# Kernel optimization log

Measured on AMD Instinct MI355X. Metric: run time of the kernel, lower is better.

Reference implementation:

```python
import jax, jax.numpy as jnp
import numpy as np

N = 50000      # nodes
E = 800000     # edges (avg degree 16)
F_IN = 512     # num_feature
H = 256        # nhid


def setup_inputs() -> dict:
    key = jax.random.key(0)
    ks = jax.random.split(key, 40)
    def p(k, shape):
        return jax.random.normal(k, shape, jnp.float32) * 0.05
    inp = {}
    inp["x"] = jax.random.normal(ks[0], (N, F_IN), jnp.float32)
    src = jax.random.randint(ks[1], (E,), 0, N, jnp.int32)
    dst = jax.random.randint(ks[2], (E,), 0, N, jnp.int32)
    inp["edge_index"] = jnp.stack([src, dst])  # [2, E]
    # GIN conv MLPs: Lin(din,H), ReLU, Lin(H,H). Weights stored [in, out].
    dims = [F_IN, H, H, H]
    i = 3
    for li, din in enumerate(dims, 1):
        inp[f"c{li}w1"] = p(ks[i], (din, H)); i += 1
        inp[f"c{li}b1"] = p(ks[i], (H,)); i += 1
        inp[f"c{li}w2"] = p(ks[i], (H, H)); i += 1
        inp[f"c{li}b2"] = p(ks[i], (H,)); i += 1
    # 2-layer LSTM, gate order i,f,g,o; single fused bias (b_ih + b_hh).
    for l in range(2):
        inp[f"lstm{l}_wih"] = p(ks[i], (H, 4 * H)); i += 1
        inp[f"lstm{l}_whh"] = p(ks[i], (H, 4 * H)); i += 1
        inp[f"lstm{l}_b"] = p(ks[i], (4 * H,)); i += 1
    inp["mlp_w"] = p(ks[i], (H, H)); i += 1
    inp["mlp_b"] = p(ks[i], (H,))
    return inp


def _gin(h, src, dst, w1, b1, w2, b2):
    # GINConv with eps=0: nn(x + sum_{j->i} x_j)
    agg = jax.ops.segment_sum(h[src], dst, num_segments=N)
    z = jax.nn.relu((h + agg) @ w1 + b1)
    return z @ w2 + b2


def _lstm_layer(seq, wih, whh, b):
    # seq: [T, N, H] -> hidden states [T, N, H]
    def step(carry, xt):
        h, c = carry
        g = xt @ wih + h @ whh + b
        i, f, gg, o = jnp.split(g, 4, axis=-1)
        c = jax.nn.sigmoid(f) * c + jax.nn.sigmoid(i) * jnp.tanh(gg)
        h = jax.nn.sigmoid(o) * jnp.tanh(c)
        return (h, c), h
    h0 = jnp.zeros((seq.shape[1], whh.shape[0]), seq.dtype)
    _, hs = jax.lax.scan(step, (h0, h0), seq)
    return hs


def reference(x, edge_index, c1w1, c1b1, c1w2, c1b2, c2w1, c2b1, c2w2, c2b2,
              c3w1, c3b1, c3w2, c3b2, c4w1, c4b1, c4w2, c4b2,
              lstm0_wih, lstm0_whh, lstm0_b, lstm1_wih, lstm1_whh, lstm1_b,
              mlp_w, mlp_b):
    src, dst = edge_index[0], edge_index[1]
    x1 = jax.nn.relu(_gin(x, src, dst, c1w1, c1b1, c1w2, c1b2))
    x2 = jax.nn.relu(_gin(x1, src, dst, c2w1, c2b1, c2w2, c2b2))
    x3 = jax.nn.relu(_gin(x2, src, dst, c3w1, c3b1, c3w2, c3b2))
    x4 = jax.nn.relu(_gin(x3, src, dst, c4w1, c4b1, c4w2, c4b2))
    # residual sums (in-place cascade as in the original)
    x2 = x2 + x1
    x3 = x3 + x2
    x4 = x4 + x3
    x_sum = x1 + x2 + x3 + x4
    stack = jnp.stack([x_sum, x1, x2, x3, x4])  # [5, N, H]
    x_avg = stack.mean(axis=0)
    x_max = stack.max(axis=0)
    seq = jnp.stack([x1, x2, x3, x4])  # [4, N, H]
    h = _lstm_layer(seq, lstm0_wih, lstm0_whh, lstm0_b)
    h = _lstm_layer(h, lstm1_wih, lstm1_whh, lstm1_b)
    x_lstm = h.mean(axis=0)
    # channel attention: relu(mlp(x_avg) + mlp(x_max) + mlp(x_lstm))
    return jax.nn.relu((x_avg + x_max + x_lstm) @ mlp_w + 3.0 * mlp_b)
```

## Files before the change

kernel.cpp:

```cpp
#include <hip/hip_runtime.h>

typedef unsigned int u32;
typedef unsigned short u16;

typedef __attribute__((ext_vector_type(8))) __bf16 bf16x8;
typedef __attribute__((ext_vector_type(4))) float f32x4;

__device__ __forceinline__ u16 f2bf(float f) {
  u32 u = __float_as_uint(f);
  u += 0x7fffu + ((u >> 16) & 1u);
  return (u16)(u >> 16);
}
__device__ __forceinline__ float bl(u32 u) { return __uint_as_float(u << 16); }
__device__ __forceinline__ float bh(u32 u) { return __uint_as_float(u & 0xffff0000u); }
__device__ __forceinline__ u32 pk2(float a, float b) { return (u32)f2bf(a) | ((u32)f2bf(b) << 16); }
__device__ __forceinline__ float fsig(float x) { return 1.f / (1.f + __expf(-x)); }
__device__ __forceinline__ float ftanh(float x) { return 1.f - 2.f / (__expf(2.f * x) + 1.f); }

#define GLDS16(gp, lp)                                                                  \
  __builtin_amdgcn_global_load_lds((const __attribute__((address_space(1))) u32*)(gp),  \
                                   (__attribute__((address_space(3))) u32*)(lp), 16, 0, 0)

struct WTargs {
  const float* src[13];
  u16* dst[13];
  int K[13];
  int Nc[13];
  int bstart[14];
};
__global__ __launch_bounds__(256) void k_wtall(WTargs wa) {
  int b = blockIdx.x;
  int w = 0;
  while (b >= wa.bstart[w + 1]) ++w;
  int i = (b - wa.bstart[w]) * 256 + threadIdx.x;
  int K = wa.K[w], Nc = wa.Nc[w];
  if (i >= K * Nc) return;
  int k = i / Nc, c = i - k * Nc;
  wa.dst[w][(size_t)c * K + k] = f2bf(wa.src[w][i]);
}

__global__ __launch_bounds__(256) void k_x2bf(const float* __restrict__ x, u16* __restrict__ xb, int total8) {
  int i = blockIdx.x * 256 + threadIdx.x;
  if (i >= total8) return;
  size_t o = (size_t)i * 8;
  float4 a = *(const float4*)(x + o), b = *(const float4*)(x + o + 4);
  uint4 v;
  v.x = pk2(a.x, a.y); v.y = pk2(a.z, a.w); v.z = pk2(b.x, b.y); v.w = pk2(b.z, b.w);
  *(uint4*)(xb + o) = v;
}

__global__ void k_hist(const int* __restrict__ dst, int* __restrict__ deg, int E) {
  int e = blockIdx.x * 256 + threadIdx.x;
  if (e < E) atomicAdd(&deg[dst[e]], 1);
}
__global__ __launch_bounds__(1024) void k_scan1(const int* __restrict__ deg, int* __restrict__ rs,
                                                int* __restrict__ bsum, int n) {
  __shared__ int buf[1024];
  int t = threadIdx.x, idx = blockIdx.x * 1024 + t;
  int v = idx < n ? deg[idx] : 0;
  buf[t] = v;
  __syncthreads();
  for (int off = 1; off < 1024; off <<= 1) {
    int u = t >= off ? buf[t - off] : 0;
    __syncthreads();
    buf[t] += u;
    __syncthreads();
  }
  if (idx < n) rs[idx + 1] = buf[t];
  if (t == 1023) bsum[blockIdx.x] = buf[1023];
}
__global__ void k_scan2(int* bsum, int nb) {
  if (threadIdx.x == 0) {
    int s = 0;
    for (int b = 0; b < nb; ++b) { s += bsum[b]; bsum[b] = s; }
  }
}
__global__ void k_scan3(const int* __restrict__ bsum, int* __restrict__ rs,
                        int* __restrict__ cursor, int n) {
  int i = blockIdx.x * 256 + threadIdx.x;
  if (i >= n) return;
  int b = i >> 10;
  int add = b ? bsum[b - 1] : 0;
  int v = rs[i + 1] + add;
  int d = cursor[i];
  rs[i + 1] = v;
  cursor[i] = v - d;
  if (i == 0) rs[0] = 0;
}
__global__ void k_scatter(const int* __restrict__ src, const int* __restrict__ dst,
                          int* __restrict__ cursor, int* __restrict__ esrc, int E) {
  int e = blockIdx.x * 256 + threadIdx.x;
  if (e < E) {
    int p = atomicAdd(&cursor[dst[e]], 1);
    esrc[p] = src[e];
  }
}

__global__ __launch_bounds__(256) void k_agg512_bf(const u16* __restrict__ xb,
                                                   const int* __restrict__ rowstart,
                                                   const int* __restrict__ esrc,
                                                   u16* __restrict__ out, int Nn, int base, int rows) {
  int lane = threadIdx.x & 63, wid = threadIdx.x >> 6;
  int r = blockIdx.x * 4 + wid;
  if (r >= rows) return;
  int node = base + r;
  const int cb = lane * 8;
  u16* orow = out + (size_t)r * 512 + cb;
  if (node >= Nn) { *(uint4*)orow = uint4{0, 0, 0, 0}; return; }
  float acc[8];
  {
    uint4 v = *(const uint4*)(xb + (size_t)node * 512 + cb);
    acc[0] = bl(v.x); acc[1] = bh(v.x); acc[2] = bl(v.y); acc[3] = bh(v.y);
    acc[4] = bl(v.z); acc[5] = bh(v.z); acc[6] = bl(v.w); acc[7] = bh(v.w);
  }
  int s = rowstart[node], e = rowstart[node + 1];
  int j = s;
  for (; j + 3 < e; j += 4) {
    uint4 v0 = *(const uint4*)(xb + (size_t)esrc[j] * 512 + cb);
    uint4 v1 = *(const uint4*)(xb + (size_t)esrc[j + 1] * 512 + cb);
    uint4 v2 = *(const uint4*)(xb + (size_t)esrc[j + 2] * 512 + cb);
    uint4 v3 = *(const uint4*)(xb + (size_t)esrc[j + 3] * 512 + cb);
    acc[0] += (bl(v0.x) + bl(v1.x)) + (bl(v2.x) + bl(v3.x));
    acc[1] += (bh(v0.x) + bh(v1.x)) + (bh(v2.x) + bh(v3.x));
    acc[2] += (bl(v0.y) + bl(v1.y)) + (bl(v2.y) + bl(v3.y));
    acc[3] += (bh(v0.y) + bh(v1.y)) + (bh(v2.y) + bh(v3.y));
    acc[4] += (bl(v0.z) + bl(v1.z)) + (bl(v2.z) + bl(v3.z));
    acc[5] += (bh(v0.z) + bh(v1.z)) + (bh(v2.z) + bh(v3.z));
    acc[6] += (bl(v0.w) + bl(v1.w)) + (bl(v2.w) + bl(v3.w));
    acc[7] += (bh(v0.w) + bh(v1.w)) + (bh(v2.w) + bh(v3.w));
  }
  for (; j < e; ++j) {
    uint4 v = *(const uint4*)(xb + (size_t)esrc[j] * 512 + cb);
    acc[0] += bl(v.x); acc[1] += bh(v.x); acc[2] += bl(v.y); acc[3] += bh(v.y);
    acc[4] += bl(v.z); acc[5] += bh(v.z); acc[6] += bl(v.w); acc[7] += bh(v.w);
  }
  uint4 o;
  o.x = pk2(acc[0], acc[1]); o.y = pk2(acc[2], acc[3]);
  o.z = pk2(acc[4], acc[5]); o.w = pk2(acc[6], acc[7]);
  *(uint4*)orow = o;
}

__global__ __launch_bounds__(256) void k_agg256(const u16* __restrict__ h,
                                                const int* __restrict__ rowstart,
                                                const int* __restrict__ esrc,
                                                u16* __restrict__ out, int Nn, int base, int rows) {
  int lane = threadIdx.x & 63, wid = threadIdx.x >> 6;
  int r = blockIdx.x * 4 + wid;
  if (r >= rows) return;
  int node = base + r;
  const int cb = lane * 4;
  u16* orow = out + (size_t)r * 256 + cb;
  if (node >= Nn) { *(uint2*)orow = uint2{0, 0}; return; }
  float acc[4];
  {
    uint2 v = *(const uint2*)(h + (size_t)node * 256 + cb);
    acc[0] = bl(v.x); acc[1] = bh(v.x); acc[2] = bl(v.y); acc[3] = bh(v.y);
  }
  int s = rowstart[node], e = rowstart[node + 1];
  int j = s;
  for (; j + 3 < e; j += 4) {
    uint2 v0 = *(const uint2*)(h + (size_t)esrc[j] * 256 + cb);
    uint2 v1 = *(const uint2*)(h + (size_t)esrc[j + 1] * 256 + cb);
    uint2 v2 = *(const uint2*)(h + (size_t)esrc[j + 2] * 256 + cb);
    uint2 v3 = *(const uint2*)(h + (size_t)esrc[j + 3] * 256 + cb);
    acc[0] += (bl(v0.x) + bl(v1.x)) + (bl(v2.x) + bl(v3.x));
    acc[1] += (bh(v0.x) + bh(v1.x)) + (bh(v2.x) + bh(v3.x));
    acc[2] += (bl(v0.y) + bl(v1.y)) + (bl(v2.y) + bl(v3.y));
    acc[3] += (bh(v0.y) + bh(v1.y)) + (bh(v2.y) + bh(v3.y));
  }
  for (; j < e; ++j) {
    uint2 v = *(const uint2*)(h + (size_t)esrc[j] * 256 + cb);
    acc[0] += bl(v.x); acc[1] += bh(v.x); acc[2] += bl(v.y); acc[3] += bh(v.y);
  }
  uint2 o;
  o.x = pk2(acc[0], acc[1]); o.y = pk2(acc[2], acc[3]);
  *(uint2*)orow = o;
}

template <int BN, int MODE>
__global__ __launch_bounds__(256) void k_gemm(const u16* __restrict__ A1, const u16* __restrict__ B1, int K1,
                                              const u16* __restrict__ A2, const u16* __restrict__ B2, int K2,
                                              const float* __restrict__ bias, float bscale,
                                              void* __restrict__ outp, int Nout, int Mstore,
                                              float* __restrict__ cstp, float* __restrict__ hsump,
                                              int first, int dosum) {
  constexpr int NF = BN / 32;
  __shared__ u16 Al[128 * 64];
  __shared__ u16 Bl[BN * 64];
  const int tid = threadIdx.x;
  const int lane = tid & 63, wid = tid >> 6;
  const int wr = wid >> 1, wc = wid & 1;
  const int m0 = blockIdx.x * 128;
  const int n0 = blockIdx.y * BN;
  const int h0 = blockIdx.y * 32;
  const int l15 = lane & 15, l4 = lane >> 4;
  const int srow = lane >> 3, scol = (lane & 7) * 8;
  f32x4 acc[4][NF] = {};

  for (int s = 0; s < 2; ++s) {
    const u16* A = s ? A2 : A1;
    const u16* B = s ? B2 : B1;
    const int K = s ? K2 : K1;
    if (A == nullptr) continue;
    for (int k0 = 0; k0 < K; k0 += 64) {
      __syncthreads();
#pragma unroll
      for (int p = 0; p < 4; ++p) {
        int r = m0 + p * 32 + wid * 8 + srow;
        GLDS16(A + (size_t)r * K + k0 + scol, &Al[(p * 32 + wid * 8) * 64]);
      }
#pragma unroll
      for (int p = 0; p < NF; ++p) {
        int r;
        if constexpr (MODE == 3) r = p * 256 + h0 + wid * 8 + srow;
        else r = n0 + p * 32 + wid * 8 + srow;
        GLDS16(B + (size_t)r * K + k0 + scol, &Bl[(p * 32 + wid * 8) * 64]);
      }
      __syncthreads();
#pragma unroll
      for (int ks = 0; ks < 2; ++ks) {
        const int kk = ks * 32 + l4 * 8;
        bf16x8 af[4], bfr[NF];
#pragma unroll
        for (int m = 0; m < 4; ++m)
          af[m] = *(const bf16x8*)&Al[(wr * 64 + m * 16 + l15) * 64 + kk];
#pragma unroll
        for (int n = 0; n < NF; ++n) {
          int trow;
          if constexpr (MODE == 3) trow = n * 32 + wc * 16 + l15;
          else trow = wc * (BN / 2) + n * 16 + l15;
          bfr[n] = *(const bf16x8*)&Bl[trow * 64 + kk];
        }
#pragma unroll
        for (int m = 0; m < 4; ++m)
#pragma unroll
          for (int n = 0; n < NF; ++n)
            acc[m][n] = __builtin_amdgcn_mfma_f32_16x16x32_bf16(af[m], bfr[n], acc[m][n], 0, 0, 0);
      }
    }
  }

  if constexpr (MODE == 3) {
    const int hcol = h0 + wc * 16 + l15;
    const float bi = bias[hcol], bf2 = bias[256 + hcol];
    const float bg = bias[512 + hcol], bo = bias[768 + hcol];
    u16* hout = (u16*)outp;
#pragma unroll
    for (int m = 0; m < 4; ++m) {
      int gr0 = m0 + wr * 64 + m * 16 + l4 * 4;
#pragma unroll
      for (int r = 0; r < 4; ++r) {
        int gr = gr0 + r;
        if (gr >= Mstore) continue;
        float gi = acc[m][0][r] + bi;
        float gf = acc[m][1][r] + bf2;
        float gg = acc[m][2][r] + bg;
        float go = acc[m][3][r] + bo;
        size_t o = (size_t)gr * 256 + hcol;
        float nc = fsig(gi) * ftanh(gg);
        if (!first) nc += fsig(gf) * cstp[o];
        cstp[o] = nc;
        float h = fsig(go) * ftanh(nc);
        hout[o] = f2bf(h);
        if (dosum) {
          if (first) hsump[o] = h;
          else hsump[o] += h;
        }
      }
    }
    return;
  }

#pragma unroll
  for (int m = 0; m < 4; ++m) {
    int gr0 = m0 + wr * 64 + m * 16 + l4 * 4;
#pragma unroll
    for (int n = 0; n < NF; ++n) {
      int gc = n0 + wc * (BN / 2) + n * 16 + l15;
      float bb = bias ? bias[gc] * bscale : 0.f;
#pragma unroll
      for (int r = 0; r < 4; ++r) {
        int gr = gr0 + r;
        if (gr >= Mstore) continue;
        float v = acc[m][n][r] + bb;
        if (MODE >= 1) v = fmaxf(v, 0.f);
        if (MODE == 2) ((float*)outp)[(size_t)gr * Nout + gc] = v;
        else ((u16*)outp)[(size_t)gr * Nout + gc] = f2bf(v);
      }
    }
  }
}

__global__ __launch_bounds__(256) void k_cascade(const u16* __restrict__ x1, u16* __restrict__ x2,
                                                 u16* __restrict__ x3, u16* __restrict__ x4, int total4) {
  int i = blockIdx.x * 256 + threadIdx.x;
  if (i >= total4) return;
  size_t o = (size_t)i * 4;
  uint2 v1 = *(const uint2*)(x1 + o), v2 = *(const uint2*)(x2 + o);
  uint2 v3 = *(const uint2*)(x3 + o), v4 = *(const uint2*)(x4 + o);
  float a1[4] = {bl(v1.x), bh(v1.x), bl(v1.y), bh(v1.y)};
  float a2[4] = {bl(v2.x), bh(v2.x), bl(v2.y), bh(v2.y)};
  float a3[4] = {bl(v3.x), bh(v3.x), bl(v3.y), bh(v3.y)};
  float a4[4] = {bl(v4.x), bh(v4.x), bl(v4.y), bh(v4.y)};
  float y2[4], y3[4], y4[4];
#pragma unroll
  for (int j = 0; j < 4; ++j) {
    y2[j] = a2[j] + a1[j];
    y3[j] = a3[j] + y2[j];
    y4[j] = a4[j] + y3[j];
  }
  *(uint2*)(x2 + o) = uint2{pk2(y2[0], y2[1]), pk2(y2[2], y2[3])};
  *(uint2*)(x3 + o) = uint2{pk2(y3[0], y3[1]), pk2(y3[2], y3[3])};
  *(uint2*)(x4 + o) = uint2{pk2(y4[0], y4[1]), pk2(y4[2], y4[3])};
}

__global__ __launch_bounds__(256) void k_sfin(const u16* __restrict__ x1, const u16* __restrict__ x2,
                                              const u16* __restrict__ x3, const u16* __restrict__ x4,
                                              const float* __restrict__ hsum, u16* __restrict__ sb,
                                              int total4) {
  int i = blockIdx.x * 256 + threadIdx.x;
  if (i >= total4) return;
  size_t o = (size_t)i * 4;
  uint2 v1 = *(const uint2*)(x1 + o), v2 = *(const uint2*)(x2 + o);
  uint2 v3 = *(const uint2*)(x3 + o), v4 = *(const uint2*)(x4 + o);
  float4 hh = *(const float4*)(hsum + o);
  float r0 = 1.4f * (bl(v1.x) + bl(v2.x) + bl(v3.x) + bl(v4.x)) + 0.25f * hh.x;
  float r1 = 1.4f * (bh(v1.x) + bh(v2.x) + bh(v3.x) + bh(v4.x)) + 0.25f * hh.y;
  float r2 = 1.4f * (bl(v1.y) + bl(v2.y) + bl(v3.y) + bl(v4.y)) + 0.25f * hh.z;
  float r3 = 1.4f * (bh(v1.y) + bh(v2.y) + bh(v3.y) + bh(v4.y)) + 0.25f * hh.w;
  *(uint2*)(sb + o) = uint2{pk2(r0, r1), pk2(r2, r3)};
}

extern "C" void kernel_launch(void* const* d_in, const int* in_sizes, int n_in,
                              void* d_out, int out_size, void* d_ws, size_t ws_size,
                              hipStream_t stream) {
  (void)n_in; (void)out_size;
  const int N = in_sizes[0] / 512;
  const int E = in_sizes[1] / 2;
  const int Mpad = ((N + 127) / 128) * 128;
  auto al128 = [](int v) { return ((v + 127) / 128) * 128; };

  const float* x = (const float*)d_in[0];
  const int* ei = (const int*)d_in[1];
  const int* esrc_in = ei;
  const int* edst_in = ei + E;

  size_t off = 0;
  auto alloc = [&](size_t bytes) { size_t o = off; off += (bytes + 255) & ~(size_t)255; return o; };
  char* ws = (char*)d_ws;
  const size_t szH = (size_t)Mpad * 256 * 2;
  const int widx[13] = {2, 4, 6, 8, 10, 12, 14, 16, 18, 19, 21, 22, 24};
  const int wK[13] = {512, 256, 256, 256, 256, 256, 256, 256, 256, 256, 256, 256, 256};
  const int wN[13] = {256, 256, 256, 256, 256, 256, 256, 256, 1024, 1024, 1024, 1024, 256};
  size_t wt_o[13];
  for (int i = 0; i < 13; ++i) wt_o[i] = alloc((size_t)wK[i] * wN[i] * 2);
  size_t rowstart_o = alloc((size_t)(N + 1) * 4);
  size_t cursor_o = alloc((size_t)N * 4);
  size_t bsum_o = alloc(256 * 4);
  size_t esrc_o = alloc((size_t)E * 4);
  size_t xb_o = alloc((size_t)Mpad * 512 * 2);
  size_t x_o[4];
  for (int t = 0; t < 4; ++t) x_o[t] = alloc(szH);
  int McC = al128((Mpad + 3) / 4);
  int McL = al128((Mpad + 7) / 8);
  {
    const int ccand[3] = {Mpad, al128((Mpad + 1) / 2), al128((Mpad + 3) / 4)};
    const int lcand[4] = {al128((Mpad + 1) / 2), 16384, 8192, al128((Mpad + 7) / 8)};
    bool done = false;
    for (int ci = 0; ci < 3 && !done; ++ci) {
      for (int li = 0; li < 4 && !done; ++li) {
        size_t cneed = (size_t)ccand[ci] * 1536;
        size_t lneed = (size_t)lcand[li] * 5632;
        size_t tmp = cneed > lneed ? cneed : lneed;
        if (off + tmp + (1u << 20) <= ws_size) { McC = ccand[ci]; McL = lcand[li]; done = true; }
      }
    }
  }
  const size_t hb = (size_t)McL * 256 * 2;
  const size_t fb = (size_t)McL * 256 * 4;
  size_t lstm_sz = 7 * hb + 2 * fb;
  size_t conv_sz = (size_t)McC * 1536;
  size_t tmp_o = alloc(lstm_sz > conv_sz ? lstm_sz : conv_sz);
  if (off > ws_size) return;

  u16* wt[13];
  for (int i = 0; i < 13; ++i) wt[i] = (u16*)(ws + wt_o[i]);
  int* rowstart = (int*)(ws + rowstart_o);
  int* cursor = (int*)(ws + cursor_o);
  int* bsum = (int*)(ws + bsum_o);
  int* esrc = (int*)(ws + esrc_o);
  u16* xb = (u16*)(ws + xb_o);
  u16* xl[4];
  for (int t = 0; t < 4; ++t) xl[t] = (u16*)(ws + x_o[t]);
  u16* h0s[4];
  for (int t = 0; t < 4; ++t) h0s[t] = (u16*)(ws + tmp_o + t * hb);
  u16* h1p[2] = {(u16*)(ws + tmp_o + 4 * hb), (u16*)(ws + tmp_o + 5 * hb)};
  float* cst = (float*)(ws + tmp_o + 6 * hb);
  float* hsum = (float*)(ws + tmp_o + 6 * hb + fb);
  u16* sbc = (u16*)(ws + tmp_o + 6 * hb + 2 * fb);
  u16* aggC = (u16*)(ws + tmp_o);
  u16* zC = (u16*)(ws + tmp_o + (size_t)McC * 512 * 2);

  WTargs wa;
  int bacc = 0;
  for (int i = 0; i < 13; ++i) {
    wa.src[i] = (const float*)d_in[widx[i]];
    wa.dst[i] = wt[i];
    wa.K[i] = wK[i];
    wa.Nc[i] = wN[i];
    wa.bstart[i] = bacc;
    bacc += (wK[i] * wN[i] + 255) / 256;
  }
  wa.bstart[13] = bacc;
  k_wtall<<<bacc, 256, 0, stream>>>(wa);
  k_x2bf<<<(N * 64 + 255) / 256, 256, 0, stream>>>(x, xb, N * 64);
  hipMemsetAsync(cursor, 0, (size_t)N * 4, stream);
  k_hist<<<(E + 255) / 256, 256, 0, stream>>>(edst_in, cursor, E);
  const int nb = (N + 1023) / 1024;
  k_scan1<<<nb, 1024, 0, stream>>>(cursor, rowstart, bsum, N);
  k_scan2<<<1, 64, 0, stream>>>(bsum, nb);
  k_scan3<<<(N + 255) / 256, 256, 0, stream>>>(bsum, rowstart, cursor, N);
  k_scatter<<<(E + 255) / 256, 256, 0, stream>>>(esrc_in, edst_in, cursor, esrc, E);

  auto gemm = [&](const u16* A1, const u16* B1, int K1, const u16* A2, const u16* B2, int K2,
                  const float* bias, float bscale, void* out, int Nout, int rows, int Mstore,
                  int mode) {
    dim3 b(256);
    if (mode == 0) {
      dim3 g(rows / 128, Nout / 128);
      k_gemm<128, 0><<<g, b, 0, stream>>>(A1, B1, K1, A2, B2, K2, bias, bscale, out, Nout, Mstore,
                                          nullptr, nullptr, 0, 0);
    } else if (mode == 1) {
      dim3 g(rows / 128, Nout / 128);
      k_gemm<128, 1><<<g, b, 0, stream>>>(A1, B1, K1, A2, B2, K2, bias, bscale, out, Nout, Mstore,
                                          nullptr, nullptr, 0, 0);
    } else {
      dim3 g(rows / 128, Nout / 64);
      k_gemm<64, 2><<<g, b, 0, stream>>>(A1, B1, K1, A2, B2, K2, bias, bscale, out, Nout, Mstore,
                                         nullptr, nullptr, 0, 0);
    }
  };
  auto lstm_step = [&](const u16* xt, const u16* wih, const u16* hprev, const u16* whh,
                       const float* bias, u16* hout, float* hsumP, int rows, int first, int dosum) {
    dim3 g(rows / 128, 8), b(256);
    k_gemm<128, 3><<<g, b, 0, stream>>>(xt, wih, 256, hprev, whh, 256, bias, 1.f,
                                        hout, 256, rows, cst, hsumP, first, dosum);
  };

  const u16* cin[4] = {nullptr, xl[0], xl[1], xl[2]};
  u16* cout[4] = {xl[0], xl[1], xl[2], xl[3]};
  const int cb1[4] = {3, 7, 11, 15}, cb2[4] = {5, 9, 13, 17};
  for (int l = 0; l < 4; ++l) {
    const int Kin = l == 0 ? 512 : 256;
    for (int base = 0; base < Mpad; base += McC) {
      int rows = Mpad - base < McC ? Mpad - base : McC;
      int ab = (rows + 3) / 4;
      if (l == 0)
        k_agg512_bf<<<ab, 256, 0, stream>>>(xb, rowstart, esrc, aggC, N, base, rows);
      else
        k_agg256<<<ab, 256, 0, stream>>>(cin[l], rowstart, esrc, aggC, N, base, rows);
      gemm(aggC, wt[2 * l], Kin, nullptr, nullptr, 0, (const float*)d_in[cb1[l]], 1.f,
           zC, 256, rows, rows, 1);
      gemm(zC, wt[2 * l + 1], 256, nullptr, nullptr, 0, (const float*)d_in[cb2[l]], 1.f,
           cout[l] + (size_t)base * 256, 256, rows, rows, 1);
    }
  }
  k_cascade<<<(Mpad * 64 + 255) / 256, 256, 0, stream>>>(xl[0], xl[1], xl[2], xl[3], Mpad * 64);

  const float* b_l0 = (const float*)d_in[20];
  const float* b_l1 = (const float*)d_in[23];
  const float* b_mlp = (const float*)d_in[25];
  for (int base = 0; base < Mpad; base += McL) {
    int rows = Mpad - base < McL ? Mpad - base : McL;
    const size_t boff = (size_t)base * 256;
    for (int t = 0; t < 4; ++t)
      lstm_step(xl[t] + boff, wt[8], t ? h0s[t - 1] : nullptr, wt[9], b_l0,
                h0s[t], nullptr, rows, t == 0, 0);
    for (int t = 0; t < 4; ++t)
      lstm_step(h0s[t], wt[10], t ? h1p[(t + 1) & 1] : nullptr, wt[11], b_l1,
                h1p[t & 1], hsum, rows, t == 0, 1);
    k_sfin<<<(rows * 64 + 255) / 256, 256, 0, stream>>>(xl[0] + boff, xl[1] + boff, xl[2] + boff,
                                                        xl[3] + boff, hsum, sbc, rows * 64);
    int st = N - base;
    if (st > rows) st = rows;
    if (st > 0)
      gemm(sbc, wt[12], 256, nullptr, nullptr, 0, b_mlp, 3.f,
           (float*)d_out + boff, 256, rows, st, 2);
  }
}
```

Measured before the change: 1.755 ms.

## Apply first GIN linear before aggregation and store LSTM cell state in bf16

Layer 1 now multiplies x by W1 first (512->256) and then aggregates the 256-wide projected features, fusing bias and ReLU into the aggregation kernel. This uses linearity of the sum to halve the gather bandwidth of the widest aggregation. Separately, the LSTM cell state is kept in bf16 instead of fp32, which halves its traffic but adds rounding error. Workspace layout is reshuffled so the bf16 copy of x lives in the temporary region, with zero padding via memset.

```diff
diff --git a/kernel.cpp b/kernel.cpp
--- a/kernel.cpp
+++ b/kernel.cpp
@@ -96,48 +96,45 @@
   }
 }
 
-__global__ __launch_bounds__(256) void k_agg512_bf(const u16* __restrict__ xb,
-                                                   const int* __restrict__ rowstart,
-                                                   const int* __restrict__ esrc,
-                                                   u16* __restrict__ out, int Nn, int base, int rows) {
+__global__ __launch_bounds__(256) void k_aggbr(const u16* __restrict__ y, const int* __restrict__ rowstart,
+                                               const int* __restrict__ esrc, const float* __restrict__ b1,
+                                               u16* __restrict__ z, int Nn, int base, int rows) {
   int lane = threadIdx.x & 63, wid = threadIdx.x >> 6;
   int r = blockIdx.x * 4 + wid;
   if (r >= rows) return;
   int node = base + r;
-  const int cb = lane * 8;
-  u16* orow = out + (size_t)r * 512 + cb;
-  if (node >= Nn) { *(uint4*)orow = uint4{0, 0, 0, 0}; return; }
-  float acc[8];
+  const int cb = lane * 4;
+  u16* orow = z + (size_t)r * 256 + cb;
+  if (node >= Nn) { *(uint2*)orow = uint2{0, 0}; return; }
+  float acc[4];
   {
-    uint4 v = *(const uint4*)(xb + (size_t)node * 512 + cb);
+    uint2 v = *(const uint2*)(y + (size_t)node * 256 + cb);
     acc[0] = bl(v.x); acc[1] = bh(v.x); acc[2] = bl(v.y); acc[3] = bh(v.y);
-    acc[4] = bl(v.z); acc[5] = bh(v.z); acc[6] = bl(v.w); acc[7] = bh(v.w);
   }
   int s = rowstart[node], e = rowstart[node + 1];
   int j = s;
   for (; j + 3 < e; j += 4) {
-    uint4 v0 = *(const uint4*)(xb + (size_t)esrc[j] * 512 + cb);
-    uint4 v1 = *(const uint4*)(xb + (size_t)esrc[j + 1] * 512 + cb);
-    uint4 v2 = *(const uint4*)(xb + (size_t)esrc[j + 2] * 512 + cb);
-    uint4 v3 = *(const uint4*)(xb + (size_t)esrc[j + 3] * 512 + cb);
+    uint2 v0 = *(const uint2*)(y + (size_t)esrc[j] * 256 + cb);
+    uint2 v1 = *(const uint2*)(y + (size_t)esrc[j + 1] * 256 + cb);
+    uint2 v2 = *(const uint2*)(y + (size_t)esrc[j + 2] * 256 + cb);
+    uint2 v3 = *(const uint2*)(y + (size_t)esrc[j + 3] * 256 + cb);
     acc[0] += (bl(v0.x) + bl(v1.x)) + (bl(v2.x) + bl(v3.x));
     acc[1] += (bh(v0.x) + bh(v1.x)) + (bh(v2.x) + bh(v3.x));
     acc[2] += (bl(v0.y) + bl(v1.y)) + (bl(v2.y) + bl(v3.y));
     acc[3] += (bh(v0.y) + bh(v1.y)) + (bh(v2.y) + bh(v3.y));
-    acc[4] += (bl(v0.z) + bl(v1.z)) + (bl(v2.z) + bl(v3.z));
-    acc[5] += (bh(v0.z) + bh(v1.z)) + (bh(v2.z) + bh(v3.z));
-    acc[6] += (bl(v0.w) + bl(v1.w)) + (bl(v2.w) + bl(v3.w));
-    acc[7] += (bh(v0.w) + bh(v1.w)) + (bh(v2.w) + bh(v3.w));
   }
   for (; j < e; ++j) {
-    uint4 v = *(const uint4*)(xb + (size_t)esrc[j] * 512 + cb);
+    uint2 v = *(const uint2*)(y + (size_t)esrc[j] * 256 + cb);
     acc[0] += bl(v.x); acc[1] += bh(v.x); acc[2] += bl(v.y); acc[3] += bh(v.y);
-    acc[4] += bl(v.z); acc[5] += bh(v.z); acc[6] += bl(v.w); acc[7] += bh(v.w);
-  }
-  uint4 o;
+  }
+  float4 bb = *(const float4*)(b1 + cb);
+  acc[0] = fmaxf(acc[0] + bb.x, 0.f);
+  acc[1] = fmaxf(acc[1] + bb.y, 0.f);
+  acc[2] = fmaxf(acc[2] + bb.z, 0.f);
+  acc[3] = fmaxf(acc[3] + bb.w, 0.f);
+  uint2 o;
   o.x = pk2(acc[0], acc[1]); o.y = pk2(acc[2], acc[3]);
-  o.z = pk2(acc[4], acc[5]); o.w = pk2(acc[6], acc[7]);
-  *(uint4*)orow = o;
+  *(uint2*)orow = o;
 }
 
 __global__ __launch_bounds__(256) void k_agg256(const u16* __restrict__ h,
@@ -182,7 +179,7 @@
                                               const u16* __restrict__ A2, const u16* __restrict__ B2, int K2,
                                               const float* __restrict__ bias, float bscale,
                                               void* __restrict__ outp, int Nout, int Mstore,
-                                              float* __restrict__ cstp, float* __restrict__ hsump,
+                                              u16* __restrict__ cstp, float* __restrict__ hsump,
                                               int first, int dosum) {
   constexpr int NF = BN / 32;
   __shared__ u16 Al[128 * 64];
@@ -258,8 +255,9 @@
         float go = acc[m][3][r] + bo;
         size_t o = (size_t)gr * 256 + hcol;
         float nc = fsig(gi) * ftanh(gg);
-        if (!first) nc += fsig(gf) * cstp[o];
-        cstp[o] = nc;
+        if (!first) nc += fsig(gf) * bl((u32)cstp[o]);
+        cstp[o] = f2bf(nc);
+        nc = bl((u32)f2bf(nc));
         float h = fsig(go) * ftanh(nc);
         hout[o] = f2bf(h);
         if (dosum) {
@@ -349,6 +347,7 @@
   auto alloc = [&](size_t bytes) { size_t o = off; off += (bytes + 255) & ~(size_t)255; return o; };
   char* ws = (char*)d_ws;
   const size_t szH = (size_t)Mpad * 256 * 2;
+  const size_t szXB = (size_t)Mpad * 512 * 2;
   const int widx[13] = {2, 4, 6, 8, 10, 12, 14, 16, 18, 19, 21, 22, 24};
   const int wK[13] = {512, 256, 256, 256, 256, 256, 256, 256, 256, 256, 256, 256, 256};
   const int wN[13] = {256, 256, 256, 256, 256, 256, 256, 256, 1024, 1024, 1024, 1024, 256};
@@ -358,7 +357,6 @@
   size_t cursor_o = alloc((size_t)N * 4);
   size_t bsum_o = alloc(256 * 4);
   size_t esrc_o = alloc((size_t)E * 4);
-  size_t xb_o = alloc((size_t)Mpad * 512 * 2);
   size_t x_o[4];
   for (int t = 0; t < 4; ++t) x_o[t] = alloc(szH);
   int McC = al128((Mpad + 3) / 4);
@@ -369,8 +367,8 @@
     bool done = false;
     for (int ci = 0; ci < 3 && !done; ++ci) {
       for (int li = 0; li < 4 && !done; ++li) {
-        size_t cneed = (size_t)ccand[ci] * 1536;
-        size_t lneed = (size_t)lcand[li] * 5632;
+        size_t cneed = szXB + szH + (size_t)ccand[ci] * 512;
+        size_t lneed = (size_t)lcand[li] * 5120;
         size_t tmp = cneed > lneed ? cneed : lneed;
         if (off + tmp + (1u << 20) <= ws_size) { McC = ccand[ci]; McL = lcand[li]; done = true; }
       }
@@ -378,8 +376,8 @@
   }
   const size_t hb = (size_t)McL * 256 * 2;
   const size_t fb = (size_t)McL * 256 * 4;
-  size_t lstm_sz = 7 * hb + 2 * fb;
-  size_t conv_sz = (size_t)McC * 1536;
+  size_t lstm_sz = 8 * hb + fb;
+  size_t conv_sz = szXB + szH + (size_t)McC * 512;
   size_t tmp_o = alloc(lstm_sz > conv_sz ? lstm_sz : conv_sz);
   if (off > ws_size) return;
 
@@ -389,17 +387,17 @@
   int* cursor = (int*)(ws + cursor_o);
   int* bsum = (int*)(ws + bsum_o);
   int* esrc = (int*)(ws + esrc_o);
-  u16* xb = (u16*)(ws + xb_o);
   u16* xl[4];
   for (int t = 0; t < 4; ++t) xl[t] = (u16*)(ws + x_o[t]);
+  u16* xb = (u16*)(ws + tmp_o);
+  u16* y1 = (u16*)(ws + tmp_o + szXB);
+  u16* zC = (u16*)(ws + tmp_o + szXB + szH);
   u16* h0s[4];
   for (int t = 0; t < 4; ++t) h0s[t] = (u16*)(ws + tmp_o + t * hb);
   u16* h1p[2] = {(u16*)(ws + tmp_o + 4 * hb), (u16*)(ws + tmp_o + 5 * hb)};
-  float* cst = (float*)(ws + tmp_o + 6 * hb);
-  float* hsum = (float*)(ws + tmp_o + 6 * hb + fb);
-  u16* sbc = (u16*)(ws + tmp_o + 6 * hb + 2 * fb);
-  u16* aggC = (u16*)(ws + tmp_o);
-  u16* zC = (u16*)(ws + tmp_o + (size_t)McC * 512 * 2);
+  u16* cst = (u16*)(ws + tmp_o + 6 * hb);
+  u16* sbc = (u16*)(ws + tmp_o + 7 * hb);
+  float* hsum = (float*)(ws + tmp_o + 8 * hb);
 
   WTargs wa;
   int bacc = 0;
@@ -414,6 +412,7 @@
   wa.bstart[13] = bacc;
   k_wtall<<<bacc, 256, 0, stream>>>(wa);
   k_x2bf<<<(N * 64 + 255) / 256, 256, 0, stream>>>(x, xb, N * 64);
+  if (Mpad > N) hipMemsetAsync(xb + (size_t)N * 512, 0, (size_t)(Mpad - N) * 512 * 2, stream);
   hipMemsetAsync(cursor, 0, (size_t)N * 4, stream);
   k_hist<<<(E + 255) / 256, 256, 0, stream>>>(edst_in, cursor, E);
   const int nb = (N + 1023) / 1024;
@@ -447,22 +446,26 @@
                                         hout, 256, rows, cst, hsumP, first, dosum);
   };
 
-  const u16* cin[4] = {nullptr, xl[0], xl[1], xl[2]};
-  u16* cout[4] = {xl[0], xl[1], xl[2], xl[3]};
-  const int cb1[4] = {3, 7, 11, 15}, cb2[4] = {5, 9, 13, 17};
-  for (int l = 0; l < 4; ++l) {
-    const int Kin = l == 0 ? 512 : 256;
+  gemm(xb, wt[0], 512, nullptr, nullptr, 0, nullptr, 0.f, y1, 256, Mpad, Mpad, 0);
+  for (int base = 0; base < Mpad; base += McC) {
+    int rows = Mpad - base < McC ? Mpad - base : McC;
+    int ab = (rows + 3) / 4;
+    k_aggbr<<<ab, 256, 0, stream>>>(y1, rowstart, esrc, (const float*)d_in[3], zC, N, base, rows);
+    gemm(zC, wt[1], 256, nullptr, nullptr, 0, (const float*)d_in[5], 1.f,
+         xl[0] + (size_t)base * 256, 256, rows, rows, 1);
+  }
+  for (int l = 1; l < 4; ++l) {
+    const int cb1[4] = {3, 7, 11, 15}, cb2[4] = {5, 9, 13, 17};
     for (int base = 0; base < Mpad; base += McC) {
       int rows = Mpad - base < McC ? Mpad - base : McC;
       int ab = (rows + 3) / 4;
-      if (l == 0)
-        k_agg512_bf<<<ab, 256, 0, stream>>>(xb, rowstart, esrc, aggC, N, base, rows);
-      else
-        k_agg256<<<ab, 256, 0, stream>>>(cin[l], rowstart, esrc, aggC, N, base, rows);
-      gemm(aggC, wt[2 * l], Kin, nullptr, nullptr, 0, (const float*)d_in[cb1[l]], 1.f,
-           zC, 256, rows, rows, 1);
-      gemm(zC, wt[2 * l + 1], 256, nullptr, nullptr, 0, (const float*)d_in[cb2[l]], 1.f,
-           cout[l] + (size_t)base * 256, 256, rows, rows, 1);
+      k_agg256<<<ab, 256, 0, stream>>>(xl[l - 1], rowstart, esrc, zC, N, base, rows);
+      (void)ab;
+      k_aggbr;
+      gemm((u16*)zC, wt[2 * l], 256, nullptr, nullptr, 0, (const float*)d_in[cb1[l]], 1.f,
+           y1, 256, rows, rows, 1);
+      gemm(y1, wt[2 * l + 1], 256, nullptr, nullptr, 0, (const float*)d_in[cb2[l]], 1.f,
+           xl[l] + (size_t)base * 256, 256, rows, rows, 1);
     }
   }
   k_cascade<<<(Mpad * 64 + 255) / 256, 256, 0, stream>>>(xl[0], xl[1], xl[2], xl[3], Mpad * 64);
```

Measured after the change: 1.693 ms. 3.5% less time.
